# Kernel optimization log

Hardware: AMD Instinct MI355X
Metric: run time of the kernel (lower is better)

Reference implementation:

```python
import jax, jax.numpy as jnp
from jax import lax
import numpy as np

B, L, N, C_IN = 32, 12, 325, 2
HID, NODE_DIM, HYP_DIM, MID_DIM, GDEP = 64, 40, 16, 2, 2
AW, BW, GW = 0.05, 0.95, 0.95   # list_weight -> alpha, beta, gamma
TA = 3.0                        # tanhalpha
DIN = (GDEP + 1) * (HID + C_IN) # gcn mlp input dim = 198


def setup_inputs() -> dict:
    key = jax.random.key(0)
    ks = jax.random.split(key, 12)
    a0 = jax.random.uniform(ks[2], (N, N), jnp.float32)
    a1 = jax.random.uniform(ks[3], (N, N), jnp.float32)
    s = 0.1
    return {
        "history_data": jax.random.normal(ks[0], (B, L, N, C_IN), jnp.float32),
        "future_data": jax.random.uniform(ks[1], (B, L, N, C_IN), jnp.float32),
        "adj_0": a0 / a0.sum(-1, keepdims=True),
        "adj_1": a1 / a1.sum(-1, keepdims=True),
        "emb1": jax.random.normal(ks[4], (N, NODE_DIM), jnp.float32) * s,
        "emb2": jax.random.normal(ks[5], (N, NODE_DIM), jnp.float32) * s,
        # 8 hyper gcns: enc{GCN1_tg, GCN1_tg_1, GCN2_tg, GCN2_tg_1}=0..3, dec versions=4..7
        "hyper_fc1_w": jax.random.normal(ks[6], (8, DIN, HYP_DIM), jnp.float32) * s,
        "hyper_fc1_b": jnp.zeros((8, HYP_DIM), jnp.float32),
        "hyper_fc2_w": jax.random.normal(ks[7], (8, HYP_DIM, MID_DIM), jnp.float32) * s,
        "hyper_fc2_b": jnp.zeros((8, MID_DIM), jnp.float32),
        "hyper_fc3_w": jax.random.normal(ks[8], (8, MID_DIM, NODE_DIM), jnp.float32) * s,
        "hyper_fc3_b": jnp.zeros((8, NODE_DIM), jnp.float32),
        # 12 RNN gcns: enc{gz1,gz2,gr1,gr2,gc1,gc2}=0..5, dec=6..11
        "rnn_w": jax.random.normal(ks[9], (12, DIN, HID), jnp.float32) * s,
        "rnn_b": jnp.zeros((12, HID), jnp.float32),
        "fc_final_w": jax.random.normal(ks[10], (HID, 1), jnp.float32) * s,
        "fc_final_b": jnp.zeros((1,), jnp.float32),
        "task_level": 12,
    }


def _hyper_gcn(x, A, w1, b1, w2, b2, w3, b3):
    # mix-hop diffusion over static A [N,N], x [B,N,F]; then sigmoid MLP -> [B,N,NODE_DIM]
    h, out = x, [x]
    for _ in range(GDEP):
        h = AW * x + GW * jnp.einsum('bvc,vw->bwc', h, A)
        out.append(h)
    ho = jnp.concatenate(out, -1)
    h1 = jax.nn.sigmoid(ho @ w1 + b1)
    h2 = jax.nn.sigmoid(h1 @ w2 + b2)
    return h2 @ w3 + b3


def _rnn_gcn(x, Adyn, Apre, w, b):
    # x [B,N,F]; Adyn [B,N,N] dynamic adjacency; Apre [N,N] predefined
    h, out = x, [x]
    for _ in range(GDEP):
        h = (AW * x + BW * jnp.einsum('bvc,bvw->bwc', h, Adyn)
             + GW * jnp.einsum('bvc,vw->bwc', h, Apre))
        out.append(h)
    return jnp.concatenate(out, -1) @ w + b


def _norm(adj):
    adj = adj + jnp.eye(adj.shape[-1], dtype=adj.dtype)
    return adj / adj.sum(-1, keepdims=True)


def _step(x, H, hy0, rb, adj_0, adj_1, emb1, emb2, hp, rnn_w, rnn_b):
    w1, b1, w2, b2, w3, b3 = hp
    hi = jnp.concatenate([x, H], -1)  # [B,N,C_IN+HID]
    hg = lambda A, i: _hyper_gcn(hi, A, w1[i], b1[i], w2[i], b2[i], w3[i], b3[i])
    f1 = hg(adj_0, hy0) + hg(adj_1, hy0 + 1)
    f2 = hg(adj_0, hy0 + 2) + hg(adj_1, hy0 + 3)
    nv1 = jnp.tanh(TA * emb1 * f1)    # [B,N,NODE_DIM]
    nv2 = jnp.tanh(TA * emb2 * f2)
    a = jnp.einsum('bid,bjd->bij', nv1, nv2)
    adj = jax.nn.relu(jnp.tanh(TA * (a - a.transpose(0, 2, 1))))
    adp = _norm(adj)
    adpT = _norm(adj.transpose(0, 2, 1))
    g = lambda inp, j: (_rnn_gcn(inp, adp, adj_0, rnn_w[rb + j], rnn_b[rb + j])
                        + _rnn_gcn(inp, adpT, adj_1, rnn_w[rb + j + 1], rnn_b[rb + j + 1]))
    z = jax.nn.sigmoid(g(hi, 0))
    r = jax.nn.sigmoid(g(hi, 2))
    temp = jnp.concatenate([x, r * H], -1)
    Cn = jnp.tanh(g(temp, 4))
    return z * H + (1.0 - z) * Cn


def _forward(history_data, future_data, adj_0, adj_1, emb1, emb2,
             hyper_fc1_w, hyper_fc1_b, hyper_fc2_w, hyper_fc2_b,
             hyper_fc3_w, hyper_fc3_b, rnn_w, rnn_b,
             fc_final_w, fc_final_b, task_level):
    b, l, n, _ = history_data.shape
    hp = (hyper_fc1_w, hyper_fc1_b, hyper_fc2_w, hyper_fc2_b, hyper_fc3_w, hyper_fc3_b)
    H0 = jnp.zeros((b, n, HID), history_data.dtype)

    def enc(H, xt):
        return _step(xt, H, 0, 0, adj_0, adj_1, emb1, emb2, hp, rnn_w, rnn_b), None
    H, _ = lax.scan(enc, H0, history_data.transpose(1, 0, 2, 3))  # [L,B,N,2] scan

    tod = future_data[:, :task_level, :, 1].transpose(1, 0, 2)  # [T,B,N] time-of-day channel

    def dec(carry, tod_t):
        H, prev = carry
        xt = jnp.stack([prev, tod_t], -1)   # [B,N,2] = [prev prediction, time-of-day]
        Hn = _step(xt, H, 4, 6, adj_0, adj_1, emb1, emb2, hp, rnn_w, rnn_b)
        out = Hn @ fc_final_w + fc_final_b  # [B,N,1]
        return (Hn, out[..., 0]), out
    _, ys = lax.scan(dec, (H, jnp.zeros((b, n), history_data.dtype)), tod)
    ys = ys.transpose(1, 0, 2, 3)           # [B,T,N,1]
    if task_level < l:
        ys = jnp.concatenate([ys, jnp.zeros((b, l - task_level, n, 1), ys.dtype)], 1)
    return ys


def reference(history_data, future_data, adj_0, adj_1, emb1, emb2,
              hyper_fc1_w, hyper_fc1_b, hyper_fc2_w, hyper_fc2_b,
              hyper_fc3_w, hyper_fc3_b, rnn_w, rnn_b,
              fc_final_w, fc_final_b, task_level):
    return _forward(history_data, future_data, adj_0, adj_1, emb1, emb2,
                    hyper_fc1_w, hyper_fc1_b, hyper_fc2_w, hyper_fc2_b,
                    hyper_fc3_w, hyper_fc3_b, rnn_w, rnn_b,
                    fc_final_w, fc_final_b, task_level)
```

## Files before the change

kernel.cpp:

```cpp
#include <hip/hip_runtime.h>

typedef unsigned short ushort_t;

constexpr int kB   = 32;
constexpr int kL   = 12;
constexpr int kN   = 325;
constexpr int kNP  = 328;
constexpr int kPc  = kB * kNP;
constexpr int kHID = 64;
constexpr int kDIN = 198;
constexpr int kND  = 40;
constexpr int kNN2 = kN * kN;
constexpr float cAW = 0.05f, cBW = 0.95f, cGW = 0.95f, cTA = 3.0f;

constexpr int kT = 192;
constexpr int kWs = 384;
constexpr int kVs = 352;
constexpr int kETb = kWs * kVs;

constexpr int kBldEV  = 1152;
constexpr int kOutU   = 164;
constexpr int kPairs  = 231;

constexpr int kKg  = 352;
constexpr int kWgN = 2 * 128 * kKg;
constexpr int kWfN = 2 * 64 * kKg;

constexpr int kInit1 = 66 * kPc;
constexpr int kInit2 = 2 * kND * kN;
constexpr int kInit3 = 2 * kETb;
constexpr int kInit4 = 4 * kB * kETb / 2;
constexpr int kInit5 = 12 * kDIN * kHID;
constexpr int kInit6 = 8 * kDIN * 16;
constexpr int kInit7 = 2 * kETb;
constexpr int kInit8 = 4 * kPc * 64 / 2;
constexpr int kInitT = kInit1 + kInit2 + kInit3 + kInit4 + kInit5 + kInit6 + kInit7 + kInit8;

using short8 = __attribute__((ext_vector_type(8))) short;
using f32x4  = __attribute__((ext_vector_type(4))) float;
union ABu { ushort_t u[8]; short8 v; };

__device__ __forceinline__ float sigm_f(float x) { return 1.f / (1.f + __expf(-x)); }
__device__ __forceinline__ float tanh_f(float x) { return 1.f - 2.f / (1.f + __expf(2.f * x)); }
__device__ __forceinline__ ushort_t f2b(float x) {
    union { float f; unsigned u; } c; c.f = x;
    unsigned r = c.u + 0x7FFFu + ((c.u >> 16) & 1u);
    return (ushort_t)(r >> 16);
}
__device__ __forceinline__ float b2f(ushort_t h) {
    union { unsigned u; float f; } c; c.u = ((unsigned)h) << 16; return c.f;
}
__device__ __forceinline__ void split_bf(float x, ushort_t& hi, ushort_t& lo) {
    hi = f2b(x);
    lo = f2b(x - b2f(hi));
}

struct KParams {
    const float *hist, *fut, *adj0, *adj1, *emb1, *emb2;
    const float *hw1, *hb1, *hw2, *hb2, *hw3, *hb3, *rnw, *rnb, *fcw, *fcb;
    float* out;
    float *xH, *hA1, *hB1, *hA2, *hB2, *tmp;
    float *zbuf, *e1T, *e2T, *rs, *cs, *adjv;
    float *a0Tf, *a1Tf;
    float *rnwC, *hw1C;
    ushort_t *E0h, *E0l, *E1h, *E1l;
    ushort_t *a0h, *a0l, *a1h, *a1l;
    ushort_t *a0Nh, *a0Nl, *a1Nh, *a1Nl;
    ushort_t *a0sh, *a0sl, *a1sh, *a1sl;
    ushort_t *Wgh, *Wgl, *Wfh, *Wfl;
    ushort_t *nv1h, *nv1l, *nv2h, *nv2l;
};

__device__ __forceinline__ void d_init(const KParams& P, int i) {
    if (i < kInit1) {
        int c = i / kPc, p = i - c * kPc;
        int b = p / kNP, n = p - b * kNP;
        if (n < kN) {
            float v = (c < 2) ? P.hist[((b * kL) * kN + n) * 2 + c] : 0.f;
            P.xH[(size_t)c * kPc + p] = v;
        }
        return;
    }
    int j = i - kInit1;
    if (j < kND * kN) { int d = j / kN, n = j - d * kN; P.e1T[j] = P.emb1[n * kND + d]; return; }
    j -= kND * kN;
    if (j < kND * kN) { int d = j / kN, n = j - d * kN; P.e2T[j] = P.emb2[n * kND + d]; return; }
    j -= kND * kN;
    if (j < kInit3) {
        int m = j / kETb, idx = j - m * kETb;
        int w = idx / kVs, v = idx - w * kVs;
        const float* adj = m ? P.adj1 : P.adj0;
        float val = (w < kN && v < kN) ? adj[(size_t)v * kN + w] : 0.f;
        ushort_t hi, lo; split_bf(val, hi, lo);
        if (m) { P.a1h[idx] = hi; P.a1l[idx] = lo; P.a1Tf[idx] = val; }
        else   { P.a0h[idx] = hi; P.a0l[idx] = lo; P.a0Tf[idx] = val; }
        return;
    }
    j -= kInit3;
    if (j < kInit4) { ((unsigned*)P.E0h)[j] = 0; return; }
    j -= kInit4;
    if (j < kInit5) {
        int m = j / (kDIN * kHID), rem = j - m * (kDIN * kHID);
        int k = rem / kHID, o = rem - k * kHID;
        const float* W = P.rnw + (size_t)m * (kDIN * kHID) + o;
        float v;
        if (k < 66)        v = W[(size_t)k * kHID] + cAW * (W[(size_t)(k + 66) * kHID] + W[(size_t)(k + 132) * kHID]);
        else if (k < 132)  v = W[(size_t)k * kHID] + cAW * W[(size_t)(k + 66) * kHID];
        else               v = W[(size_t)k * kHID];
        P.rnwC[j] = v;
        return;
    }
    j -= kInit5;
    if (j < kInit6) {
        int m = j / (kDIN * 16), rem = j - m * (kDIN * 16);
        int k = rem / 16, o = rem - k * 16;
        const float* W = P.hw1 + (size_t)m * (kDIN * 16) + o;
        float v;
        if (k < 66)        v = W[(size_t)k * 16] + cAW * (W[(size_t)(k + 66) * 16] + W[(size_t)(k + 132) * 16]);
        else if (k < 132)  v = cGW * (W[(size_t)k * 16] + cAW * W[(size_t)(k + 66) * 16]);
        else               v = cGW * cGW * W[(size_t)k * 16];
        P.hw1C[j] = v;
        return;
    }
    j -= kInit6;
    if (j < kInit7) {
        int m = j / kETb, idx = j - m * kETb;
        int v = idx / kVs, u = idx - v * kVs;
        const float* adj = m ? P.adj1 : P.adj0;
        float val = (v < kN && u < kN) ? adj[(size_t)v * kN + u] : 0.f;
        ushort_t hi, lo; split_bf(val, hi, lo);
        if (m) { P.a1Nh[idx] = hi; P.a1Nl[idx] = lo; }
        else   { P.a0Nh[idx] = hi; P.a0Nl[idx] = lo; }
        return;
    }
    j -= kInit7;
    if (j < kInit8) ((unsigned*)P.nv1h)[j] = 0;
}
__global__ __launch_bounds__(kT) void g_init(KParams P) {
    const int gtid = blockIdx.x * kT + threadIdx.x;
    const int nt = gridDim.x * kT;
    for (int i = gtid; i < kInitT; i += nt) d_init(P, i);
}

__global__ __launch_bounds__(kT) void g_init2(KParams P) {
    const int tot = kWgN + kWfN;
    for (int i = blockIdx.x * kT + threadIdx.x; i < tot; i += gridDim.x * kT) {
        bool isG = i < kWgN;
        int j = isG ? i : i - kWgN;
        int Mloc = isG ? 128 : 64;
        int g = j / (Mloc * kKg);
        int rem = j - g * (Mloc * kKg);
        int m = rem / kKg, k = rem - m * kKg;
        int rbg = g ? 6 : 0;
        int base0, base1, h;
        if (isG) {
            if (m < 64) { base0 = rbg + 0; base1 = rbg + 1; h = m; }
            else        { base0 = rbg + 2; base1 = rbg + 3; h = m - 64; }
        } else { base0 = rbg + 4; base1 = rbg + 5; h = m; }
        float w = 0.f;
        if (k < 66)
            w = P.rnwC[(size_t)base0 * (kDIN * kHID) + k * kHID + h]
              + P.rnwC[(size_t)base1 * (kDIN * kHID) + k * kHID + h];
        else if (k < 198)
            w = P.rnwC[(size_t)base0 * (kDIN * kHID) + k * kHID + h];
        else if (k < 330)
            w = P.rnwC[(size_t)base1 * (kDIN * kHID) + (k - 132) * kHID + h];
        ushort_t hi, lo; split_bf(w, hi, lo);
        if (isG) { P.Wgh[j] = hi; P.Wgl[j] = lo; }
        else     { P.Wfh[j] = hi; P.Wfl[j] = lo; }
    }
}

__global__ __launch_bounds__(64) void g_esq(KParams P) {
    const int lane = threadIdx.x;
    const int quad = lane >> 4, ln15 = lane & 15;
    const int m0 = blockIdx.x * 16, n0 = blockIdx.y * 16;
    const int mat = blockIdx.z;
    const ushort_t* STh = mat ? P.a1h : P.a0h;
    const ushort_t* STl = mat ? P.a1l : P.a0l;
    const ushort_t* SNh = mat ? P.a1Nh : P.a0Nh;
    const ushort_t* SNl = mat ? P.a1Nl : P.a0Nl;
    ushort_t* Oh = mat ? P.a1sh : P.a0sh;
    ushort_t* Ol = mat ? P.a1sl : P.a0sl;
    const size_t arow = (size_t)(m0 + ln15) * kVs + quad * 8;
    const size_t browq = (size_t)(n0 + ln15) * kVs + quad * 8;
    f32x4 acc = f32x4{0.f, 0.f, 0.f, 0.f};
    for (int ks = 0; ks < 11; ++ks) {
        const int u0 = ks * 32;
        ABu ah, al, bh, bl;
        ah.v = *(const short8*)(STh + arow + u0);
        al.v = *(const short8*)(STl + arow + u0);
        bh.v = *(const short8*)(SNh + browq + u0);
        bl.v = *(const short8*)(SNl + browq + u0);
        acc = __builtin_amdgcn_mfma_f32_16x16x32_bf16(ah.v, bh.v, acc, 0, 0, 0);
        acc = __builtin_amdgcn_mfma_f32_16x16x32_bf16(al.v, bh.v, acc, 0, 0, 0);
        acc = __builtin_amdgcn_mfma_f32_16x16x32_bf16(ah.v, bl.v, acc, 0, 0, 0);
    }
#pragma unroll
    for (int r = 0; r < 4; ++r) {
        size_t o = (size_t)(m0 + quad * 4 + r) * kVs + n0 + ln15;
        ushort_t hi, lo; split_bf(acc[r], hi, lo);
        Oh[o] = hi; Ol[o] = lo;
    }
}

__device__ __forceinline__ void hop_tile(
        const ushort_t* __restrict__ EH, const ushort_t* __restrict__ EL,
        const float* __restrict__ ap, const size_t* brow, f32x4* acc) {
    for (int ks = 0; ks < 11; ++ks) {
        const int v0 = ks * 32;
        float4 f0 = *(const float4*)(ap + v0);
        float4 f1 = *(const float4*)(ap + v0 + 4);
        float fs[8] = {f0.x, f0.y, f0.z, f0.w, f1.x, f1.y, f1.z, f1.w};
        ABu ah, al;
#pragma unroll
        for (int j = 0; j < 8; ++j) {
            ushort_t hi = f2b(fs[j]);
            ah.u[j] = hi;
            al.u[j] = f2b(fs[j] - b2f(hi));
        }
#pragma unroll
        for (int nn = 0; nn < 4; ++nn) {
            short8 bh = *(const short8*)(EH + brow[nn] + v0);
            short8 bl = *(const short8*)(EL + brow[nn] + v0);
            acc[nn] = __builtin_amdgcn_mfma_f32_16x16x32_bf16(ah.v, bh, acc[nn], 0, 0, 0);
            acc[nn] = __builtin_amdgcn_mfma_f32_16x16x32_bf16(al.v, bh, acc[nn], 0, 0, 0);
            acc[nn] = __builtin_amdgcn_mfma_f32_16x16x32_bf16(ah.v, bl, acc[nn], 0, 0, 0);
        }
    }
}

__global__ __launch_bounds__(320) void g_hyper(KParams P) {
    const int lane = threadIdx.x & 63;
    const int ct = threadIdx.x >> 6;
    const int quad = lane >> 4, ln15 = lane & 15;
    const int w0 = blockIdx.x * 64;
    const int zb = blockIdx.y;
    const int hop = zb >> 6;
    const int z = zb & 63;
    const int sel = z >> 5, b = z & 31;
    const ushort_t* EH = hop ? (sel ? P.a1sh : P.a0sh) : (sel ? P.a1h : P.a0h);
    const ushort_t* EL = hop ? (sel ? P.a1sl : P.a0sl) : (sel ? P.a1l : P.a0l);
    float* ob = (hop ? (sel ? P.hB2 : P.hA2) : (sel ? P.hB1 : P.hA1)) + b * kNP;
    const float* ap = P.xH + b * kNP + (size_t)(ct * 16 + ln15) * kPc + quad * 8;
    size_t brow[4];
#pragma unroll
    for (int nn = 0; nn < 4; ++nn)
        brow[nn] = (size_t)(w0 + nn * 16 + ln15) * kVs + quad * 8;
    f32x4 acc[4];
#pragma unroll
    for (int nn = 0; nn < 4; ++nn) acc[nn] = f32x4{0.f, 0.f, 0.f, 0.f};
    hop_tile(EH, EL, ap, brow, acc);
#pragma unroll
    for (int nn = 0; nn < 4; ++nn) {
        int w = w0 + nn * 16 + ln15;
        if (w < kN) {
#pragma unroll
            for (int r = 0; r < 4; ++r) {
                int c = ct * 16 + quad * 4 + r;
                if (c < 66) ob[(size_t)c * kPc + w] = acc[nn][r];
            }
        }
    }
}

__global__ __launch_bounds__(320) void g_hopm(
        const ushort_t* __restrict__ MaH, const ushort_t* __restrict__ MaL,
        const ushort_t* __restrict__ MbH, const ushort_t* __restrict__ MbL,
        int mstride,
        const float* __restrict__ hA, const float* __restrict__ hB,
        float* __restrict__ oA, float* __restrict__ oB) {
    const int lane = threadIdx.x & 63;
    const int ct = threadIdx.x >> 6;
    const int quad = lane >> 4, ln15 = lane & 15;
    const int w0 = blockIdx.x * 64;
    const int zb = blockIdx.y;
    const int sel = zb >> 5, b = zb & 31;
    const ushort_t* EH = (sel ? MbH : MaH) + (size_t)b * mstride;
    const ushort_t* EL = (sel ? MbL : MaL) + (size_t)b * mstride;
    const float* hb = (sel ? hB : hA) + b * kNP;
    float* ob = (sel ? oB : oA) + b * kNP;
    const float* ap = hb + (size_t)(ct * 16 + ln15) * kPc + quad * 8;
    size_t brow[4];
#pragma unroll
    for (int nn = 0; nn < 4; ++nn)
        brow[nn] = (size_t)(w0 + nn * 16 + ln15) * kVs + quad * 8;
    f32x4 acc[4];
#pragma unroll
    for (int nn = 0; nn < 4; ++nn) acc[nn] = f32x4{0.f, 0.f, 0.f, 0.f};
    hop_tile(EH, EL, ap, brow, acc);
#pragma unroll
    for (int nn = 0; nn < 4; ++nn) {
        int w = w0 + nn * 16 + ln15;
        if (w < kN) {
#pragma unroll
            for (int r = 0; r < 4; ++r) {
                int c = ct * 16 + quad * 4 + r;
                if (c < 66) ob[(size_t)c * kPc + w] = acc[nn][r];
            }
        }
    }
}

__global__ __launch_bounds__(512) void g_gatesm(KParams P, int g, int rb) {
    __shared__ ushort_t Bh[2][32][40];
    __shared__ ushort_t Bl[2][32][40];
    const int t = threadIdx.x;
    const int lane = t & 63;
    const int wv = t >> 6;
    const int quad = lane >> 4, ln15 = lane & 15;
    const int p0 = blockIdx.x * 32;
    const float* segp[5] = {P.xH, P.hA1, P.hA2, P.hB1, P.hB2};
    const int m = wv * 16 + ln15;
    const ushort_t* Ah = P.Wgh + ((size_t)(g * 128 + m)) * kKg + quad * 8;
    const ushort_t* Al = P.Wgl + ((size_t)(g * 128 + m)) * kKg + quad * 8;

    f32x4 acc[2];
    acc[0] = f32x4{0.f, 0.f, 0.f, 0.f};
    acc[1] = f32x4{0.f, 0.f, 0.f, 0.f};

    auto stage = [&](int bi, int ks) {
#pragma unroll
        for (int e = 0; e < 2; ++e) {
            int idx = e * 512 + t;
            int k = idx >> 5, n = idx & 31;
            int kg = ks * 32 + k;
            float v = 0.f;
            if (kg < 330) {
                int seg = kg / 66, row = kg - seg * 66;
                v = segp[seg][(size_t)row * kPc + p0 + n];
            }
            ushort_t hi, lo; split_bf(v, hi, lo);
            Bh[bi][n][k] = hi; Bl[bi][n][k] = lo;
        }
    };
    stage(0, 0);
    __syncthreads();
    for (int ks = 0; ks < 11; ++ks) {
        const int bi = ks & 1;
        ABu ah, al;
        ah.v = *(const short8*)(Ah + ks * 32);
        al.v = *(const short8*)(Al + ks * 32);
#pragma unroll
        for (int nt = 0; nt < 2; ++nt) {
            ABu bh, bl;
            bh.v = *(const short8*)&Bh[bi][nt * 16 + ln15][quad * 8];
            bl.v = *(const short8*)&Bl[bi][nt * 16 + ln15][quad * 8];
            acc[nt] = __builtin_amdgcn_mfma_f32_16x16x32_bf16(ah.v, bh.v, acc[nt], 0, 0, 0);
            acc[nt] = __builtin_amdgcn_mfma_f32_16x16x32_bf16(al.v, bh.v, acc[nt], 0, 0, 0);
            acc[nt] = __builtin_amdgcn_mfma_f32_16x16x32_bf16(ah.v, bl.v, acc[nt], 0, 0, 0);
        }
        if (ks + 1 < 11) stage((ks + 1) & 1, ks + 1);
        __syncthreads();
    }
#pragma unroll
    for (int nt = 0; nt < 2; ++nt) {
        int p = p0 + nt * 16 + ln15;
#pragma unroll
        for (int r = 0; r < 4; ++r) {
            int mm = wv * 16 + quad * 4 + r;
            float v = acc[nt][r];
            if (mm < 64) {
                int h = mm;
                float bz = P.rnb[(rb + 0) * kHID + h] + P.rnb[(rb + 1) * kHID + h];
                P.zbuf[(size_t)h * kPc + p] = sigm_f(v + bz);
            } else {
                int h = mm - 64;
                float br = P.rnb[(rb + 2) * kHID + h] + P.rnb[(rb + 3) * kHID + h];
                float rr = sigm_f(v + br);
                P.tmp[(size_t)(2 + h) * kPc + p] = rr * P.xH[(size_t)(2 + h) * kPc + p];
            }
        }
    }
    if (wv == 0 && quad == 0) {
#pragma unroll
        for (int nt = 0; nt < 2; ++nt) {
            int p = p0 + nt * 16 + ln15;
            P.tmp[p] = P.xH[p];
            P.tmp[kPc + p] = P.xH[kPc + p];
        }
    }
}

__global__ __launch_bounds__(256) void g_finalm(KParams P, int g, int rb, int t_, int nextmode) {
    __shared__ ushort_t Bh[2][32][40];
    __shared__ ushort_t Bl[2][32][40];
    const int t = threadIdx.x;
    const int lane = t & 63;
    const int wv = t >> 6;
    const int quad = lane >> 4, ln15 = lane & 15;
    const int p0 = blockIdx.x * 32;
    const float* segp[5] = {P.tmp, P.hA1, P.hA2, P.hB1, P.hB2};
    const int m = wv * 16 + ln15;
    const ushort_t* Ah = P.Wfh + ((size_t)(g * 64 + m)) * kKg + quad * 8;
    const ushort_t* Al = P.Wfl + ((size_t)(g * 64 + m)) * kKg + quad * 8;

    f32x4 acc[2];
    acc[0] = f32x4{0.f, 0.f, 0.f, 0.f};
    acc[1] = f32x4{0.f, 0.f, 0.f, 0.f};

    auto stage = [&](int bi, int ks) {
#pragma unroll
        for (int e = 0; e < 4; ++e) {
            int idx = e * 256 + t;
            int k = idx >> 5, n = idx & 31;
            int kg = ks * 32 + k;
            float v = 0.f;
            if (kg < 330) {
                int seg = kg / 66, row = kg - seg * 66;
                v = segp[seg][(size_t)row * kPc + p0 + n];
            }
            ushort_t hi, lo; split_bf(v, hi, lo);
            Bh[bi][n][k] = hi; Bl[bi][n][k] = lo;
        }
    };
    stage(0, 0);
    __syncthreads();
    for (int ks = 0; ks < 11; ++ks) {
        const int bi = ks & 1;
        ABu ah, al;
        ah.v = *(const short8*)(Ah + ks * 32);
        al.v = *(const short8*)(Al + ks * 32);
#pragma unroll
        for (int nt = 0; nt < 2; ++nt) {
            ABu bh, bl;
            bh.v = *(const short8*)&Bh[bi][nt * 16 + ln15][quad * 8];
            bl.v = *(const short8*)&Bl[bi][nt * 16 + ln15][quad * 8];
            acc[nt] = __builtin_amdgcn_mfma_f32_16x16x32_bf16(ah.v, bh.v, acc[nt], 0, 0, 0);
            acc[nt] = __builtin_amdgcn_mfma_f32_16x16x32_bf16(al.v, bh.v, acc[nt], 0, 0, 0);
            acc[nt] = __builtin_amdgcn_mfma_f32_16x16x32_bf16(ah.v, bl.v, acc[nt], 0, 0, 0);
        }
        if (ks + 1 < 11) stage((ks + 1) & 1, ks + 1);
        __syncthreads();
    }
#pragma unroll
    for (int nt = 0; nt < 2; ++nt) {
        int p = p0 + nt * 16 + ln15;
#pragma unroll
        for (int r = 0; r < 4; ++r) {
            int h = wv * 16 + quad * 4 + r;
            float bc = P.rnb[(rb + 4) * kHID + h] + P.rnb[(rb + 5) * kHID + h];
            float cn = tanh_f(acc[nt][r] + bc);
            float zz = P.zbuf[(size_t)h * kPc + p];
            size_t hidx = (size_t)(2 + h) * kPc + p;
            float hv = P.xH[hidx];
            P.xH[hidx] = zz * hv + (1.f - zz) * cn;
        }
    }
    if (wv == 0 && quad == 0 && nextmode != 2) {
#pragma unroll
        for (int nt = 0; nt < 2; ++nt) {
            int p = p0 + nt * 16 + ln15;
            int b = p / kNP, n = p - b * kNP;
            if (n < kN) {
                float r0, r1;
                if (nextmode == 0) {
                    r0 = P.hist[((b * kL + (t_ + 1)) * kN + n) * 2 + 0];
                    r1 = P.hist[((b * kL + (t_ + 1)) * kN + n) * 2 + 1];
                } else {
                    r0 = 0.f;
                    r1 = P.fut[((b * kL + 0) * kN + n) * 2 + 1];
                }
                P.xH[p] = r0;
                P.xH[kPc + p] = r1;
            }
        }
    }
}

__global__ __launch_bounds__(768) void g_mlp(KParams P, int hy0) {
    {
        int zt = blockIdx.x * 768 + threadIdx.x;
        if (zt < kB * kN) P.rs[zt] = 0.f;
        else if (zt < 2 * kB * kN) P.cs[zt - kB * kN] = 0.f;
    }
    __shared__ float part[12][16][64];
    __shared__ float s2s[4][2][64];
    const int lane = threadIdx.x & 63;
    const int wv = threadIdx.x >> 6;
    const int p = blockIdx.x * 64 + lane;
    const int m = wv & 3, s = wv >> 2;
    const int ig = hy0 + m;
    const float* src = (s == 0) ? P.xH : (s == 1) ? ((m & 1) ? P.hB1 : P.hA1)
                                                  : ((m & 1) ? P.hB2 : P.hA2);
    const float* wp = P.hw1C + (size_t)ig * (kDIN * 16);
    float acc[16];
#pragma unroll
    for (int o = 0; o < 16; ++o) acc[o] = 0.f;
#pragma unroll 2
    for (int kl = 0; kl < 66; ++kl) {
        int kk = s * 66 + kl;
        float u = src[(size_t)kl * kPc + p];
        float4 wa = *(const float4*)(wp + kk * 16);
        float4 wb = *(const float4*)(wp + kk * 16 + 4);
        float4 wc = *(const float4*)(wp + kk * 16 + 8);
        float4 wd = *(const float4*)(wp + kk * 16 + 12);
        acc[0]  = fmaf(u, wa.x, acc[0]);  acc[1]  = fmaf(u, wa.y, acc[1]);
        acc[2]  = fmaf(u, wa.z, acc[2]);  acc[3]  = fmaf(u, wa.w, acc[3]);
        acc[4]  = fmaf(u, wb.x, acc[4]);  acc[5]  = fmaf(u, wb.y, acc[5]);
        acc[6]  = fmaf(u, wb.z, acc[6]);  acc[7]  = fmaf(u, wb.w, acc[7]);
        acc[8]  = fmaf(u, wc.x, acc[8]);  acc[9]  = fmaf(u, wc.y, acc[9]);
        acc[10] = fmaf(u, wc.z, acc[10]); acc[11] = fmaf(u, wc.w, acc[11]);
        acc[12] = fmaf(u, wd.x, acc[12]); acc[13] = fmaf(u, wd.y, acc[13]);
        acc[14] = fmaf(u, wd.z, acc[14]); acc[15] = fmaf(u, wd.w, acc[15]);
    }
#pragma unroll
    for (int o = 0; o < 16; ++o) part[wv][o][lane] = acc[o];
    __syncthreads();
    if (wv < 4) {
        int mm = wv, igm = hy0 + mm;
        float sv[16];
#pragma unroll
        for (int o = 0; o < 16; ++o)
            sv[o] = sigm_f(P.hb1[igm * 16 + o] + part[mm][o][lane] + part[4 + mm][o][lane] + part[8 + mm][o][lane]);
#pragma unroll
        for (int j = 0; j < 2; ++j) {
            float t = P.hb2[igm * 2 + j];
#pragma unroll
            for (int o = 0; o < 16; ++o) t = fmaf(sv[o], P.hw2[igm * 32 + o * 2 + j], t);
            s2s[mm][j][lane] = sigm_f(t);
        }
    }
    __syncthreads();
    int b = p / kNP, n = p - b * kNP;
    int nc = (n < kN) ? n : (kN - 1);
    bool ok = (n < kN);
    if (wv < 2) {
        int i0 = hy0 + wv * 2;
        float sa0 = s2s[wv * 2 + 0][0][lane], sa1 = s2s[wv * 2 + 0][1][lane];
        float sb0 = s2s[wv * 2 + 1][0][lane], sb1 = s2s[wv * 2 + 1][1][lane];
        const float* eT = wv ? P.e2T : P.e1T;
        ushort_t* nvh = wv ? P.nv2h : P.nv1h;
        ushort_t* nvl = wv ? P.nv2l : P.nv1l;
#pragma unroll 4
        for (int d = 0; d < kND; ++d) {
            float f = P.hb3[(i0 + 0) * kND + d] + P.hb3[(i0 + 1) * kND + d]
                    + sa0 * P.hw3[(i0 + 0) * 80 + d] + sa1 * P.hw3[(i0 + 0) * 80 + 40 + d]
                    + sb0 * P.hw3[(i0 + 1) * 80 + d] + sb1 * P.hw3[(i0 + 1) * 80 + 40 + d];
            float r = tanh_f(cTA * eT[d * kN + nc] * f);
            if (ok) {
                ushort_t hi, lo; split_bf(r, hi, lo);
                nvh[(size_t)p * 64 + d] = hi;
                nvl[(size_t)p * 64 + d] = lo;
            }
        }
    }
}

__global__ __launch_bounds__(64) void g_adjm(KParams P) {
    __shared__ float c2t[16][17];
    const int b = blockIdx.y;
    int ti = 0, rem = blockIdx.x;
    while (rem >= 21 - ti) { rem -= 21 - ti; ++ti; }
    const int tj = ti + rem;
    const int i0 = ti * 16, j0 = tj * 16;
    const int lane = threadIdx.x, quad = lane >> 4, ln15 = lane & 15;
    const size_t pb = (size_t)b * kNP;
    auto rowoff = [&](int n) {
        int ncl = (n < kNP) ? n : (kNP - 1);
        return (pb + ncl) * 64 + quad * 8;
    };
    const size_t aI = rowoff(i0 + ln15);
    const size_t aJ = rowoff(j0 + ln15);

    f32x4 c1 = f32x4{0.f, 0.f, 0.f, 0.f};
    f32x4 c2 = f32x4{0.f, 0.f, 0.f, 0.f};
#pragma unroll
    for (int ks = 0; ks < 2; ++ks) {
        const int k0 = ks * 32;
        ABu a1h, a1l, b1h, b1l, a2h, a2l, b2h, b2l;
        a1h.v = *(const short8*)(P.nv1h + aI + k0);
        a1l.v = *(const short8*)(P.nv1l + aI + k0);
        b1h.v = *(const short8*)(P.nv2h + aJ + k0);
        b1l.v = *(const short8*)(P.nv2l + aJ + k0);
        c1 = __builtin_amdgcn_mfma_f32_16x16x32_bf16(a1h.v, b1h.v, c1, 0, 0, 0);
        c1 = __builtin_amdgcn_mfma_f32_16x16x32_bf16(a1l.v, b1h.v, c1, 0, 0, 0);
        c1 = __builtin_amdgcn_mfma_f32_16x16x32_bf16(a1h.v, b1l.v, c1, 0, 0, 0);
        a2h.v = *(const short8*)(P.nv1h + aJ + k0);
        a2l.v = *(const short8*)(P.nv1l + aJ + k0);
        b2h.v = *(const short8*)(P.nv2h + aI + k0);
        b2l.v = *(const short8*)(P.nv2l + aI + k0);
        c2 = __builtin_amdgcn_mfma_f32_16x16x32_bf16(a2h.v, b2h.v, c2, 0, 0, 0);
        c2 = __builtin_amdgcn_mfma_f32_16x16x32_bf16(a2l.v, b2h.v, c2, 0, 0, 0);
        c2 = __builtin_amdgcn_mfma_f32_16x16x32_bf16(a2h.v, b2l.v, c2, 0, 0, 0);
    }
#pragma unroll
    for (int r = 0; r < 4; ++r) c2t[quad * 4 + r][ln15] = c2[r];
    __syncthreads();

    size_t base = (size_t)b * kNN2;
    const bool diag = (ti == tj);
    float v1[4], v2[4];
#pragma unroll
    for (int r = 0; r < 4; ++r) {
        int i = i0 + quad * 4 + r;
        int j = j0 + ln15;
        float aji = c2t[ln15][quad * 4 + r];
        float tv = tanh_f(cTA * (c1[r] - aji));
        bool valid = (i < kN) && (j < kN);
        v1[r] = valid ? fmaxf(tv, 0.f) : 0.f;
        v2[r] = valid ? fmaxf(-tv, 0.f) : 0.f;
        if (valid) {
            P.adjv[base + (size_t)i * kN + j] = v1[r];
            if (!diag) P.adjv[base + (size_t)j * kN + i] = v2[r];
        }
    }
#pragma unroll
    for (int r = 0; r < 4; ++r) {
        float sr = v1[r];
#pragma unroll
        for (int off = 1; off < 16; off <<= 1) sr += __shfl_xor(sr, off);
        int i = i0 + quad * 4 + r;
        if (ln15 == 0 && i < kN) atomicAdd(&P.rs[b * kN + i], sr);
    }
    {
        float pc = v1[0] + v1[1] + v1[2] + v1[3];
        pc += __shfl_xor(pc, 16);
        pc += __shfl_xor(pc, 32);
        int j = j0 + ln15;
        if (quad == 0 && j < kN) atomicAdd(&P.cs[b * kN + j], pc);
    }
    if (!diag) {
        {
            float pr = v2[0] + v2[1] + v2[2] + v2[3];
            pr += __shfl_xor(pr, 16);
            pr += __shfl_xor(pr, 32);
            int j = j0 + ln15;
            if (quad == 0 && j < kN) atomicAdd(&P.rs[b * kN + j], pr);
        }
#pragma unroll
        for (int r = 0; r < 4; ++r) {
            float sc = v2[r];
#pragma unroll
            for (int off = 1; off < 16; off <<= 1) sc += __shfl_xor(sc, off);
            int i = i0 + quad * 4 + r;
            if (ln15 == 0 && i < kN) atomicAdd(&P.cs[b * kN + i], sc);
        }
    }
}

__global__ __launch_bounds__(kT) void g_buildE(KParams P) {
    __shared__ float tA[64][65];
    __shared__ float tB[64][65];
    for (int vb = blockIdx.x; vb < kBldEV; vb += gridDim.x) {
        const int lane = threadIdx.x & 63;
        const int wv = threadIdx.x >> 6;
        const int w0 = (vb % 6) * 64;
        const int v0 = ((vb / 6) % 6) * 64;
        const int b = vb / 36;
        const float* av = P.adjv + (size_t)b * kNN2;
        for (int r = wv; r < 64; r += 3) {
            int v = v0 + r, w = w0 + lane;
            tA[r][lane] = (v < kN && w < kN) ? av[(size_t)v * kN + w] : 0.f;
            int v2 = w0 + r, w2 = v0 + lane;
            tB[r][lane] = (v2 < kN && w2 < kN) ? av[(size_t)v2 * kN + w2] : 0.f;
        }
        __syncthreads();
        for (int r = wv; r < 64; r += 3) {
            int w = w0 + r;
            int v = v0 + lane;
            if (w < kN && v < kN) {
                size_t o = ((size_t)b * kWs + w) * kVs + v;
                float dlt = (v == w) ? 1.f : 0.f;
                {
                    float iv = 1.f / (1.f + P.rs[b * kN + v]);
                    float e = cBW * (tA[lane][r] + dlt) * iv + cGW * P.a0Tf[(size_t)w * kVs + v];
                    ushort_t hi, lo; split_bf(e, hi, lo);
                    P.E0h[o] = hi; P.E0l[o] = lo;
                }
                {
                    float iv = 1.f / (1.f + P.cs[b * kN + v]);
                    float e = cBW * (tB[r][lane] + dlt) * iv + cGW * P.a1Tf[(size_t)w * kVs + v];
                    ushort_t hi, lo; split_bf(e, hi, lo);
                    P.E1h[o] = hi; P.E1l[o] = lo;
                }
            }
        }
        __syncthreads();
    }
}

__global__ __launch_bounds__(kT) void g_out(KParams P, int t) {
    const int lane = threadIdx.x & 63;
    const int gw = blockIdx.x * 3 + (threadIdx.x >> 6);
    const int nw = gridDim.x * 3;
    for (int u = gw; u < kOutU; u += nw) {
        const int p = u * 64 + lane;
        const int b = p / kNP, n = p - b * kNP;
        if (n >= kN) continue;
        float acc = P.fcb[0];
#pragma unroll
        for (int h = 0; h < kHID; ++h) acc = fmaf(P.xH[(size_t)(2 + h) * kPc + p], P.fcw[h], acc);
        P.out[(b * 12 + t) * kN + n] = acc;
        if (t + 1 < 12) {
            P.xH[p] = acc;
            P.xH[kPc + p] = P.fut[((b * kL + (t + 1)) * kN + n) * 2 + 1];
        }
    }
}

extern "C" void kernel_launch(void* const* d_in, const int* in_sizes, int n_in,
                              void* d_out, int out_size, void* d_ws, size_t ws_size,
                              hipStream_t stream) {
    KParams P;
    P.hist = (const float*)d_in[0];
    P.fut  = (const float*)d_in[1];
    P.adj0 = (const float*)d_in[2];
    P.adj1 = (const float*)d_in[3];
    P.emb1 = (const float*)d_in[4];
    P.emb2 = (const float*)d_in[5];
    P.hw1  = (const float*)d_in[6];
    P.hb1  = (const float*)d_in[7];
    P.hw2  = (const float*)d_in[8];
    P.hb2  = (const float*)d_in[9];
    P.hw3  = (const float*)d_in[10];
    P.hb3  = (const float*)d_in[11];
    P.rnw  = (const float*)d_in[12];
    P.rnb  = (const float*)d_in[13];
    P.fcw  = (const float*)d_in[14];
    P.fcb  = (const float*)d_in[15];
    P.out  = (float*)d_out;

    float* ws = (float*)d_ws;
    const size_t SEG = (size_t)66 * kPc;
    size_t off = 0;
    P.xH   = ws + off; off += SEG;
    P.hA1  = ws + off; off += SEG;
    P.hB1  = ws + off; off += SEG;
    P.hA2  = ws + off; off += SEG;
    P.hB2  = ws + off; off += SEG;
    P.tmp  = ws + off; off += SEG;
    P.zbuf = ws + off; off += (size_t)64 * kPc;
    P.e1T  = ws + off; off += kND * kN;
    P.e2T  = ws + off; off += kND * kN;
    P.rs   = ws + off; off += kB * kN;
    P.cs   = ws + off; off += kB * kN;
    P.adjv = ws + off; off += (size_t)kB * kNN2;
    P.a0Tf = ws + off; off += kETb;
    P.a1Tf = ws + off; off += kETb;
    P.rnwC = ws + off; off += (size_t)12 * kDIN * kHID;
    P.hw1C = ws + off; off += (size_t)8 * kDIN * 16;
    P.E0h  = (ushort_t*)(ws + off); off += (size_t)kB * kETb / 2;
    P.E0l  = (ushort_t*)(ws + off); off += (size_t)kB * kETb / 2;
    P.E1h  = (ushort_t*)(ws + off); off += (size_t)kB * kETb / 2;
    P.E1l  = (ushort_t*)(ws + off); off += (size_t)kB * kETb / 2;
    P.a0h  = (ushort_t*)(ws + off); off += kETb / 2;
    P.a0l  = (ushort_t*)(ws + off); off += kETb / 2;
    P.a1h  = (ushort_t*)(ws + off); off += kETb / 2;
    P.a1l  = (ushort_t*)(ws + off); off += kETb / 2;
    P.a0Nh = (ushort_t*)(ws + off); off += kETb / 2;
    P.a0Nl = (ushort_t*)(ws + off); off += kETb / 2;
    P.a1Nh = (ushort_t*)(ws + off); off += kETb / 2;
    P.a1Nl = (ushort_t*)(ws + off); off += kETb / 2;
    P.a0sh = (ushort_t*)(ws + off); off += kETb / 2;
    P.a0sl = (ushort_t*)(ws + off); off += kETb / 2;
    P.a1sh = (ushort_t*)(ws + off); off += kETb / 2;
    P.a1sl = (ushort_t*)(ws + off); off += kETb / 2;
    P.Wgh  = (ushort_t*)(ws + off); off += kWgN / 2;
    P.Wgl  = (ushort_t*)(ws + off); off += kWgN / 2;
    P.Wfh  = (ushort_t*)(ws + off); off += kWfN / 2;
    P.Wfl  = (ushort_t*)(ws + off); off += kWfN / 2;
    P.nv1h = (ushort_t*)(ws + off); off += (size_t)kPc * 64 / 2;
    P.nv1l = (ushort_t*)(ws + off); off += (size_t)kPc * 64 / 2;
    P.nv2h = (ushort_t*)(ws + off); off += (size_t)kPc * 64 / 2;
    P.nv2l = (ushort_t*)(ws + off); off += (size_t)kPc * 64 / 2;

    g_init<<<dim3(1024), dim3(kT), 0, stream>>>(P);
    g_init2<<<dim3(704), dim3(kT), 0, stream>>>(P);
    g_esq<<<dim3(24, 22, 2), dim3(64), 0, stream>>>(P);

    for (int step = 0; step < 24; ++step) {
        const int dec = step >= 12;
        const int t = dec ? step - 12 : step;
        const int hy0 = dec ? 4 : 0;
        const int rb = dec ? 6 : 0;
        const int nextmode = dec ? 2 : (step == 11 ? 1 : 0);

        g_hyper<<<dim3(6, 128), dim3(320), 0, stream>>>(P);
        g_mlp<<<dim3(kPc / 64), dim3(768), 0, stream>>>(P, hy0);
        g_adjm<<<dim3(kPairs, kB), dim3(64), 0, stream>>>(P);
        g_buildE<<<dim3(kBldEV), dim3(kT), 0, stream>>>(P);

        g_hopm<<<dim3(6, 64), dim3(320), 0, stream>>>(P.E0h, P.E0l, P.E1h, P.E1l, kETb,
                                                      P.xH, P.xH, P.hA1, P.hB1);
        g_hopm<<<dim3(6, 64), dim3(320), 0, stream>>>(P.E0h, P.E0l, P.E1h, P.E1l, kETb,
                                                      P.hA1, P.hB1, P.hA2, P.hB2);
        g_gatesm<<<dim3(kPc / 32), dim3(512), 0, stream>>>(P, dec, rb);

        g_hopm<<<dim3(6, 64), dim3(320), 0, stream>>>(P.E0h, P.E0l, P.E1h, P.E1l, kETb,
                                                      P.tmp, P.tmp, P.hA1, P.hB1);
        g_hopm<<<dim3(6, 64), dim3(320), 0, stream>>>(P.E0h, P.E0l, P.E1h, P.E1l, kETb,
                                                      P.hA1, P.hB1, P.hA2, P.hB2);
        g_finalm<<<dim3(kPc / 32), dim3(256), 0, stream>>>(P, dec, rb, t, nextmode);

        if (dec) g_out<<<dim3(55), dim3(kT), 0, stream>>>(P, t);
    }
    (void)in_sizes; (void)n_in; (void)out_size; (void)ws_size;
}
```

Measured before the change: 7.427 ms.

## Precompute squared propagation matrix per batch and fuse two hops into one launch

Each step now also writes the transposed propagation matrix and forms its square with a per-batch MFMA GEMM (g_esq2). Both diffusion hops can then be computed directly from the input in a single g_hop2x launch instead of two dependent hop launches per gate. The fc_final output projection is folded into g_finalm through a shared-memory reduction, which removes the separate g_out kernel. The cost is an extra batched 352x352 GEMM, doubled E storage and write traffic each step, and slightly different rounding because the hi/lo bf16 split is applied to the squared matrix.

Result: slower. 9.944 ms (+33.9%).

```diff
diff --git a/kernel.cpp b/kernel.cpp
--- a/kernel.cpp
+++ b/kernel.cpp
@@ -19,7 +19,6 @@
 constexpr int kETb = kWs * kVs;
 
 constexpr int kBldEV  = 1152;
-constexpr int kOutU   = 164;
 constexpr int kPairs  = 231;
 
 constexpr int kKg  = 352;
@@ -29,7 +28,7 @@
 constexpr int kInit1 = 66 * kPc;
 constexpr int kInit2 = 2 * kND * kN;
 constexpr int kInit3 = 2 * kETb;
-constexpr int kInit4 = 4 * kB * kETb / 2;
+constexpr int kInit4 = 8 * kB * kETb / 2;
 constexpr int kInit5 = 12 * kDIN * kHID;
 constexpr int kInit6 = 8 * kDIN * 16;
 constexpr int kInit7 = 2 * kETb;
@@ -64,6 +63,8 @@
     float *a0Tf, *a1Tf;
     float *rnwC, *hw1C;
     ushort_t *E0h, *E0l, *E1h, *E1l;
+    ushort_t *EN0h, *EN0l, *EN1h, *EN1l;
+    ushort_t *S0h, *S0l, *S1h, *S1l;
     ushort_t *a0h, *a0l, *a1h, *a1l;
     ushort_t *a0Nh, *a0Nl, *a1Nh, *a1Nl;
     ushort_t *a0sh, *a0sl, *a1sh, *a1sl;
@@ -204,6 +205,40 @@
     }
 }
 
+__global__ __launch_bounds__(64) void g_esq2(KParams P) {
+    const int lane = threadIdx.x;
+    const int quad = lane >> 4, ln15 = lane & 15;
+    const int m0 = blockIdx.x * 16, n0 = blockIdx.y * 16;
+    const int z = blockIdx.z;
+    const int ch = z >> 5, b = z & 31;
+    const ushort_t* Ah = (ch ? P.E1h : P.E0h) + (size_t)b * kETb;
+    const ushort_t* Al = (ch ? P.E1l : P.E0l) + (size_t)b * kETb;
+    const ushort_t* Bh = (ch ? P.EN1h : P.EN0h) + (size_t)b * kETb;
+    const ushort_t* Bl = (ch ? P.EN1l : P.EN0l) + (size_t)b * kETb;
+    ushort_t* Oh = (ch ? P.S1h : P.S0h) + (size_t)b * kETb;
+    ushort_t* Ol = (ch ? P.S1l : P.S0l) + (size_t)b * kETb;
+    const size_t arow = (size_t)(m0 + ln15) * kVs + quad * 8;
+    const size_t brow = (size_t)(n0 + ln15) * kVs + quad * 8;
+    f32x4 acc = f32x4{0.f, 0.f, 0.f, 0.f};
+    for (int ks = 0; ks < 11; ++ks) {
+        const int v0 = ks * 32;
+        ABu ah, al, bh, bl;
+        ah.v = *(const short8*)(Ah + arow + v0);
+        al.v = *(const short8*)(Al + arow + v0);
+        bh.v = *(const short8*)(Bh + brow + v0);
+        bl.v = *(const short8*)(Bl + brow + v0);
+        acc = __builtin_amdgcn_mfma_f32_16x16x32_bf16(ah.v, bh.v, acc, 0, 0, 0);
+        acc = __builtin_amdgcn_mfma_f32_16x16x32_bf16(al.v, bh.v, acc, 0, 0, 0);
+        acc = __builtin_amdgcn_mfma_f32_16x16x32_bf16(ah.v, bl.v, acc, 0, 0, 0);
+    }
+#pragma unroll
+    for (int r = 0; r < 4; ++r) {
+        size_t o = (size_t)(m0 + quad * 4 + r) * kVs + n0 + ln15;
+        ushort_t hi, lo; split_bf(acc[r], hi, lo);
+        Oh[o] = hi; Ol[o] = lo;
+    }
+}
+
 __device__ __forceinline__ void hop_tile(
         const ushort_t* __restrict__ EH, const ushort_t* __restrict__ EL,
         const float* __restrict__ ap, const size_t* brow, f32x4* acc) {
@@ -264,23 +299,19 @@
     }
 }
 
-__global__ __launch_bounds__(320) void g_hopm(
-        const ushort_t* __restrict__ MaH, const ushort_t* __restrict__ MaL,
-        const ushort_t* __restrict__ MbH, const ushort_t* __restrict__ MbL,
-        int mstride,
-        const float* __restrict__ hA, const float* __restrict__ hB,
-        float* __restrict__ oA, float* __restrict__ oB) {
+__global__ __launch_bounds__(320) void g_hop2x(KParams P, const float* __restrict__ src) {
     const int lane = threadIdx.x & 63;
     const int ct = threadIdx.x >> 6;
     const int quad = lane >> 4, ln15 = lane & 15;
     const int w0 = blockIdx.x * 64;
     const int zb = blockIdx.y;
-    const int sel = zb >> 5, b = zb & 31;
-    const ushort_t* EH = (sel ? MbH : MaH) + (size_t)b * mstride;
-    const ushort_t* EL = (sel ? MbL : MaL) + (size_t)b * mstride;
-    const float* hb = (sel ? hB : hA) + b * kNP;
-    float* ob = (sel ? oB : oA) + b * kNP;
-    const float* ap = hb + (size_t)(ct * 16 + ln15) * kPc + quad * 8;
+    const int hop = zb >> 6;
+    const int z = zb & 63;
+    const int sel = z >> 5, b = z & 31;
+    const ushort_t* EH = (hop ? (sel ? P.S1h : P.S0h) : (sel ? P.E1h : P.E0h)) + (size_t)b * kETb;
+    const ushort_t* EL = (hop ? (sel ? P.S1l : P.S0l) : (sel ? P.E1l : P.E0l)) + (size_t)b * kETb;
+    float* ob = (hop ? (sel ? P.hB2 : P.hA2) : (sel ? P.hB1 : P.hA1)) + b * kNP;
+    const float* ap = src + b * kNP + (size_t)(ct * 16 + ln15) * kPc + quad * 8;
     size_t brow[4];
 #pragma unroll
     for (int nn = 0; nn < 4; ++nn)
@@ -385,6 +416,7 @@
 __global__ __launch_bounds__(256) void g_finalm(KParams P, int g, int rb, int t_, int nextmode) {
     __shared__ ushort_t Bh[2][32][40];
     __shared__ ushort_t Bl[2][32][40];
+    __shared__ float sred[16][33];
     const int t = threadIdx.x;
     const int lane = t & 63;
     const int wv = t >> 6;
@@ -433,6 +465,7 @@
         if (ks + 1 < 11) stage((ks + 1) & 1, ks + 1);
         __syncthreads();
     }
+    float pout[2] = {0.f, 0.f};
 #pragma unroll
     for (int nt = 0; nt < 2; ++nt) {
         int p = p0 + nt * 16 + ln15;
@@ -444,25 +477,49 @@
             float zz = P.zbuf[(size_t)h * kPc + p];
             size_t hidx = (size_t)(2 + h) * kPc + p;
             float hv = P.xH[hidx];
-            P.xH[hidx] = zz * hv + (1.f - zz) * cn;
-        }
-    }
-    if (wv == 0 && quad == 0 && nextmode != 2) {
-#pragma unroll
-        for (int nt = 0; nt < 2; ++nt) {
-            int p = p0 + nt * 16 + ln15;
+            float hn = zz * hv + (1.f - zz) * cn;
+            P.xH[hidx] = hn;
+            pout[nt] = fmaf(P.fcw[h], hn, pout[nt]);
+        }
+    }
+    if (nextmode != 2) {
+        if (wv == 0 && quad == 0) {
+#pragma unroll
+            for (int nt = 0; nt < 2; ++nt) {
+                int p = p0 + nt * 16 + ln15;
+                int b = p / kNP, n = p - b * kNP;
+                if (n < kN) {
+                    float r0, r1;
+                    if (nextmode == 0) {
+                        r0 = P.hist[((b * kL + (t_ + 1)) * kN + n) * 2 + 0];
+                        r1 = P.hist[((b * kL + (t_ + 1)) * kN + n) * 2 + 1];
+                    } else {
+                        r0 = 0.f;
+                        r1 = P.fut[((b * kL + 0) * kN + n) * 2 + 1];
+                    }
+                    P.xH[p] = r0;
+                    P.xH[kPc + p] = r1;
+                }
+            }
+        }
+    } else {
+#pragma unroll
+        for (int nt = 0; nt < 2; ++nt)
+            sred[wv * 4 + quad][nt * 16 + ln15] = pout[nt];
+        __syncthreads();
+        if (t < 32) {
+            int col = t;
+            float s = P.fcb[0];
+#pragma unroll
+            for (int q = 0; q < 16; ++q) s += sred[q][col];
+            int p = p0 + col;
             int b = p / kNP, n = p - b * kNP;
             if (n < kN) {
-                float r0, r1;
-                if (nextmode == 0) {
-                    r0 = P.hist[((b * kL + (t_ + 1)) * kN + n) * 2 + 0];
-                    r1 = P.hist[((b * kL + (t_ + 1)) * kN + n) * 2 + 1];
-                } else {
-                    r0 = 0.f;
-                    r1 = P.fut[((b * kL + 0) * kN + n) * 2 + 1];
+                P.out[(b * 12 + t_) * kN + n] = s;
+                if (t_ + 1 < 12) {
+                    P.xH[p] = s;
+                    P.xH[kPc + p] = P.fut[((b * kL + (t_ + 1)) * kN + n) * 2 + 1];
                 }
-                P.xH[p] = r0;
-                P.xH[kPc + p] = r1;
             }
         }
     }
@@ -642,6 +699,7 @@
 __global__ __launch_bounds__(kT) void g_buildE(KParams P) {
     __shared__ float tA[64][65];
     __shared__ float tB[64][65];
+    __shared__ float tE[64][65];
     for (int vb = blockIdx.x; vb < kBldEV; vb += gridDim.x) {
         const int lane = threadIdx.x & 63;
         const int wv = threadIdx.x >> 6;
@@ -657,45 +715,53 @@
         }
         __syncthreads();
         for (int r = wv; r < 64; r += 3) {
-            int w = w0 + r;
-            int v = v0 + lane;
+            int w = w0 + r, v = v0 + lane;
+            float e = 0.f;
             if (w < kN && v < kN) {
+                float dlt = (v == w) ? 1.f : 0.f;
+                float iv = 1.f / (1.f + P.rs[b * kN + v]);
+                e = cBW * (tA[lane][r] + dlt) * iv + cGW * P.a0Tf[(size_t)w * kVs + v];
                 size_t o = ((size_t)b * kWs + w) * kVs + v;
+                ushort_t hi, lo; split_bf(e, hi, lo);
+                P.E0h[o] = hi; P.E0l[o] = lo;
+            }
+            tE[r][lane] = e;
+        }
+        __syncthreads();
+        for (int r = wv; r < 64; r += 3) {
+            int v = v0 + r, w = w0 + lane;
+            if (v < kN && w < kN) {
+                float e = tE[lane][r];
+                size_t o = ((size_t)b * kWs + v) * kVs + w;
+                ushort_t hi, lo; split_bf(e, hi, lo);
+                P.EN0h[o] = hi; P.EN0l[o] = lo;
+            }
+        }
+        __syncthreads();
+        for (int r = wv; r < 64; r += 3) {
+            int w = w0 + r, v = v0 + lane;
+            float e = 0.f;
+            if (w < kN && v < kN) {
                 float dlt = (v == w) ? 1.f : 0.f;
-                {
-                    float iv = 1.f / (1.f + P.rs[b * kN + v]);
-                    float e = cBW * (tA[lane][r] + dlt) * iv + cGW * P.a0Tf[(size_t)w * kVs + v];
-                    ushort_t hi, lo; split_bf(e, hi, lo);
-                    P.E0h[o] = hi; P.E0l[o] = lo;
-                }
-                {
-                    float iv = 1.f / (1.f + P.cs[b * kN + v]);
-                    float e = cBW * (tB[r][lane] + dlt) * iv + cGW * P.a1Tf[(size_t)w * kVs + v];
-                    ushort_t hi, lo; split_bf(e, hi, lo);
-                    P.E1h[o] = hi; P.E1l[o] = lo;
-                }
-            }
+                float iv = 1.f / (1.f + P.cs[b * kN + v]);
+                e = cBW * (tB[r][lane] + dlt) * iv + cGW * P.a1Tf[(size_t)w * kVs + v];
+                size_t o = ((size_t)b * kWs + w) * kVs + v;
+                ushort_t hi, lo; split_bf(e, hi, lo);
+                P.E1h[o] = hi; P.E1l[o] = lo;
+            }
+            tE[r][lane] = e;
         }
         __syncthreads();
-    }
-}
-
-__global__ __launch_bounds__(kT) void g_out(KParams P, int t) {
-    const int lane = threadIdx.x & 63;
-    const int gw = blockIdx.x * 3 + (threadIdx.x >> 6);
-    const int nw = gridDim.x * 3;
-    for (int u = gw; u < kOutU; u += nw) {
-        const int p = u * 64 + lane;
-        const int b = p / kNP, n = p - b * kNP;
-        if (n >= kN) continue;
-        float acc = P.fcb[0];
-#pragma unroll
-        for (int h = 0; h < kHID; ++h) acc = fmaf(P.xH[(size_t)(2 + h) * kPc + p], P.fcw[h], acc);
-        P.out[(b * 12 + t) * kN + n] = acc;
-        if (t + 1 < 12) {
-            P.xH[p] = acc;
-            P.xH[kPc + p] = P.fut[((b * kL + (t + 1)) * kN + n) * 2 + 1];
-        }
+        for (int r = wv; r < 64; r += 3) {
+            int v = v0 + r, w = w0 + lane;
+            if (v < kN && w < kN) {
+                float e = tE[lane][r];
+                size_t o = ((size_t)b * kWs + v) * kVs + w;
+                ushort_t hi, lo; split_bf(e, hi, lo);
+                P.EN1h[o] = hi; P.EN1l[o] = lo;
+            }
+        }
+        __syncthreads();
     }
 }
 
@@ -744,6 +810,14 @@
     P.E0l  = (ushort_t*)(ws + off); off += (size_t)kB * kETb / 2;
     P.E1h  = (ushort_t*)(ws + off); off += (size_t)kB * kETb / 2;
     P.E1l  = (ushort_t*)(ws + off); off += (size_t)kB * kETb / 2;
+    P.EN0h = (ushort_t*)(ws + off); off += (size_t)kB * kETb / 2;
+    P.EN0l = (ushort_t*)(ws + off); off += (size_t)kB * kETb / 2;
+    P.EN1h = (ushort_t*)(ws + off); off += (size_t)kB * kETb / 2;
+    P.EN1l = (ushort_t*)(ws + off); off += (size_t)kB * kETb / 2;
+    P.S0h  = (ushort_t*)(ws + off); off += (size_t)kB * kETb / 2;
+    P.S0l  = (ushort_t*)(ws + off); off += (size_t)kB * kETb / 2;
+    P.S1h  = (ushort_t*)(ws + off); off += (size_t)kB * kETb / 2;
+    P.S1l  = (ushort_t*)(ws + off); off += (size_t)kB * kETb / 2;
     P.a0h  = (ushort_t*)(ws + off); off += kETb / 2;
     P.a0l  = (ushort_t*)(ws + off); off += kETb / 2;
     P.a1h  = (ushort_t*)(ws + off); off += kETb / 2;
@@ -780,20 +854,13 @@
         g_mlp<<<dim3(kPc / 64), dim3(768), 0, stream>>>(P, hy0);
         g_adjm<<<dim3(kPairs, kB), dim3(64), 0, stream>>>(P);
         g_buildE<<<dim3(kBldEV), dim3(kT), 0, stream>>>(P);
-
-        g_hopm<<<dim3(6, 64), dim3(320), 0, stream>>>(P.E0h, P.E0l, P.E1h, P.E1l, kETb,
-                                                      P.xH, P.xH, P.hA1, P.hB1);
-        g_hopm<<<dim3(6, 64), dim3(320), 0, stream>>>(P.E0h, P.E0l, P.E1h, P.E1l, kETb,
-                                                      P.hA1, P.hB1, P.hA2, P.hB2);
+        g_esq2<<<dim3(24, 22, 64), dim3(64), 0, stream>>>(P);
+
+        g_hop2x<<<dim3(6, 128), dim3(320), 0, stream>>>(P, P.xH);
         g_gatesm<<<dim3(kPc / 32), dim3(512), 0, stream>>>(P, dec, rb);
 
-        g_hopm<<<dim3(6, 64), dim3(320), 0, stream>>>(P.E0h, P.E0l, P.E1h, P.E1l, kETb,
-                                                      P.tmp, P.tmp, P.hA1, P.hB1);
-        g_hopm<<<dim3(6, 64), dim3(320), 0, stream>>>(P.E0h, P.E0l, P.E1h, P.E1l, kETb,
-                                                      P.hA1, P.hB1, P.hA2, P.hB2);
+        g_hop2x<<<dim3(6, 128), dim3(320), 0, stream>>>(P, P.tmp);
         g_finalm<<<dim3(kPc / 32), dim3(256), 0, stream>>>(P, dec, rb, t, nextmode);
-
-        if (dec) g_out<<<dim3(55), dim3(kT), 0, stream>>>(P, t);
     }
     (void)in_sizes; (void)n_in; (void)out_size; (void)ws_size;
 }
```
